# Performance work log

Hardware: AMD Instinct MI355X
Metric: run time of the kernel (lower is better)

The kernel has to match this reference:

```python
import jax, jax.numpy as jnp
import numpy as np

B, S, H = 64, 256, 1024


def setup_inputs() -> dict:
    key = jax.random.key(0)
    ks = jax.random.split(key, 16)
    f32 = jnp.float32

    def xavier(k, fan_in, fan_out):
        s = (2.0 / (fan_in + fan_out)) ** 0.5
        return jax.random.normal(k, (fan_in, fan_out), f32) * s

    return {
        "D": jax.random.normal(ks[0], (B, S, H), f32),
        "Q": jax.random.normal(ks[1], (B, 1, H), f32),
        "prev_mem": jax.random.normal(ks[2], (B, 1, H), f32),
        # AttnGRUCell params (weights stored [in, out])
        "Wr": xavier(ks[3], H, H), "br": jnp.zeros((H,), f32),
        "Ur": xavier(ks[4], H, H), "bur": jnp.zeros((H,), f32),
        "Wx": xavier(ks[5], H, H), "bx": jnp.zeros((H,), f32),
        "U": xavier(ks[6], H, H), "bu": jnp.zeros((H,), f32),
        # gate MLP
        "W1": xavier(ks[7], 4 * H, H), "b1": jnp.zeros((H,), f32),
        "W2": xavier(ks[8], H, 1), "b2": jnp.zeros((1,), f32),
        # memory update
        "Wm": xavier(ks[9], 3 * H, H), "bm": jnp.zeros((H,), f32),
    }


def reference(D, Q, prev_mem, Wr, br, Ur, bur, Wx, bx, U, bu, W1, b1, W2, b2, Wm, bm):
    # ----- gateMatrix: attention gate over sentences -----
    # z: [B, S, 4H]
    z = jnp.concatenate([D * Q, D * prev_mem, jnp.abs(D - Q), jnp.abs(D - prev_mem)], axis=-1)
    Zs = jnp.tanh(z @ W1 + b1) @ W2 + b2          # [B, S, 1]
    G = jax.nn.softmax(Zs[..., 0], axis=1)        # [B, S]

    # ----- AttnGRU: precompute input projections, scan over sentences -----
    Dr = D @ Wr + br                               # [B, S, H]
    Dw = D @ Wx + bx                               # [B, S, H]

    def step(h, t):
        dr, dw, g = t                              # dr,dw: [B,H]; g: [B]
        r = jax.nn.sigmoid(dr + h @ Ur + bur)
        h_tilda = jnp.tanh(dw + r * (h @ U + bu))
        g = g[:, None]
        h_new = g * h_tilda + (1.0 - g) * h
        return h_new, h_new

    h0 = jnp.zeros((D.shape[0], Ur.shape[0]), D.dtype)
    xs = (jnp.swapaxes(Dr, 0, 1), jnp.swapaxes(Dw, 0, 1), G.T)  # time-major
    C, hs = jax.lax.scan(step, h0, xs)
    hs = jnp.swapaxes(hs, 0, 1)                    # [B, S, H]

    # ----- memory update (dropout is identity in eval mode) -----
    concat = jnp.concatenate([prev_mem[:, 0, :], C, Q[:, 0, :]], axis=-1)  # [B, 3H]
    next_mem = jax.nn.relu(concat @ Wm + bm)[:, None, :]                    # [B, 1, H]
    return next_mem, hs
```

## Files before the change

### kernel.cpp

```cpp
#include <hip/hip_runtime.h>
#include <stdint.h>

typedef __bf16 bf16x8 __attribute__((ext_vector_type(8)));
typedef float f32x4 __attribute__((ext_vector_type(4)));

__device__ __forceinline__ float bf2f(unsigned short h) {
    union { unsigned int u; float f; } v; v.u = ((unsigned int)h) << 16; return v.f;
}
__device__ __forceinline__ unsigned short f2bf(float f) {
    union { float f; unsigned int u; } v; v.f = f;
    unsigned int r = (v.u + 0x7FFFu + ((v.u >> 16) & 1u)) >> 16;
    return (unsigned short)r;
}
__device__ __forceinline__ unsigned short f2bf_trunc(float f) {
    union { float f; unsigned int u; } v; v.f = f;
    return (unsigned short)(v.u >> 16);
}
__device__ __forceinline__ bf16x8 ldfrag(const unsigned short* p) {
    uint4 u = *(const uint4*)p; return __builtin_bit_cast(bf16x8, u);
}
__device__ __forceinline__ bf16x8 ldfrag_coh(const unsigned short* p) {
    union { unsigned long long q[2]; bf16x8 v; } u;
    u.q[0] = __hip_atomic_load((const unsigned long long*)p, __ATOMIC_RELAXED, __HIP_MEMORY_SCOPE_AGENT);
    u.q[1] = __hip_atomic_load((const unsigned long long*)(p + 4), __ATOMIC_RELAXED, __HIP_MEMORY_SCOPE_AGENT);
    return u.v;
}
__device__ __forceinline__ float fsigm(float x) { return 1.f / (1.f + __expf(-x)); }
__device__ __forceinline__ float ftanh(float x) { float e = __expf(2.f * x); return 1.f - 2.f / (e + 1.f); }

__global__ __launch_bounds__(256) void k_cast(const float* __restrict__ src,
                                              unsigned short* __restrict__ dst, int n4) {
    int i = blockIdx.x * 256 + threadIdx.x;
    if (i >= n4) return;
    float4 v = ((const float4*)src)[i];
    union { unsigned short s[4]; uint2 u; } o;
    o.s[0] = f2bf(v.x); o.s[1] = f2bf(v.y); o.s[2] = f2bf(v.z); o.s[3] = f2bf(v.w);
    ((uint2*)dst)[i] = o.u;
}

__global__ __launch_bounds__(256) void k_transpose_bf16(const float* __restrict__ src,
                                                        unsigned short* __restrict__ dst,
                                                        int R, int C) {
    __shared__ float tile[32][33];
    int tc = threadIdx.x & 31, tr = threadIdx.x >> 5;
    int r0 = blockIdx.y * 32, c0 = blockIdx.x * 32;
#pragma unroll
    for (int p = 0; p < 4; p++) tile[tr + p * 8][tc] = src[(size_t)(r0 + tr + p * 8) * C + c0 + tc];
    __syncthreads();
#pragma unroll
    for (int p = 0; p < 4; p++) dst[(size_t)(c0 + tr + p * 8) * R + r0 + tc] = f2bf(tile[tc][tr + p * 8]);
}

__global__ __launch_bounds__(256, 2) void k_gemm1(
    const unsigned short* __restrict__ Dc, const unsigned short* __restrict__ Qc,
    const unsigned short* __restrict__ Pc, const unsigned short* __restrict__ W1t,
    const float* __restrict__ b1, const float* __restrict__ W2, float* __restrict__ Zpart) {
    __shared__ alignas(16) unsigned short As[128][40];
    __shared__ alignas(16) unsigned short Bs[256][40];
    __shared__ float red[128];
    const int tid = threadIdx.x;
    const int nt = blockIdx.x, mt = blockIdx.y;
    const int r0 = mt * 128, n0 = nt * 256, b = r0 >> 8;
    const int lane = tid & 63, wid = tid >> 6;
    const int qm = wid & 1, qn = wid >> 1;
    const int nlane = lane & 15, quad = lane >> 4, k0 = quad * 8;

    f32x4 acc[4][8];
#pragma unroll
    for (int im = 0; im < 4; im++)
#pragma unroll
        for (int in = 0; in < 8; in++) acc[im][in] = (f32x4){0.f, 0.f, 0.f, 0.f};

    for (int kt = 0; kt < 128; ++kt) {
        const int q = kt >> 5;
        const int kq = (kt & 31) * 32;
        const unsigned short* wsrc = (q & 1) ? Pc : Qc;
#pragma unroll
        for (int rep = 0; rep < 2; ++rep) {
            int c = tid + rep * 256;
            int row = c >> 2, part = c & 3;
            uint4 d8 = *(const uint4*)(Dc + (size_t)(r0 + row) * 1024 + kq + part * 8);
            uint4 w8 = *(const uint4*)(wsrc + (size_t)b * 1024 + kq + part * 8);
            const unsigned short* d16 = (const unsigned short*)&d8;
            const unsigned short* w16 = (const unsigned short*)&w8;
            uint4 o; unsigned short* o16 = (unsigned short*)&o;
#pragma unroll
            for (int j = 0; j < 8; j++) {
                float dv = bf2f(d16[j]), wv = bf2f(w16[j]);
                float r = (q < 2) ? dv * wv : fabsf(dv - wv);
                o16[j] = f2bf_trunc(r);
            }
            *(uint4*)&As[row][part * 8] = o;
        }
#pragma unroll
        for (int rep = 0; rep < 4; ++rep) {
            int c = tid + rep * 256;
            int n = c >> 2, part = c & 3;
            *(uint4*)&Bs[n][part * 8] =
                *(const uint4*)(W1t + (size_t)(n0 + n) * 4096 + kt * 32 + part * 8);
        }
        __syncthreads();
        bf16x8 af[4], bfr[8];
#pragma unroll
        for (int im = 0; im < 4; im++) af[im] = ldfrag(&As[qm * 64 + im * 16 + nlane][k0]);
#pragma unroll
        for (int in = 0; in < 8; in++) bfr[in] = ldfrag(&Bs[qn * 128 + in * 16 + nlane][k0]);
#pragma unroll
        for (int im = 0; im < 4; im++)
#pragma unroll
            for (int in = 0; in < 8; in++)
                acc[im][in] = __builtin_amdgcn_mfma_f32_16x16x32_bf16(af[im], bfr[in], acc[im][in], 0, 0, 0);
        __syncthreads();
    }
    if (tid < 128) red[tid] = 0.f;
    __syncthreads();
    float b1v[8], w2v[8];
#pragma unroll
    for (int in = 0; in < 8; in++) {
        int col = n0 + qn * 128 + in * 16 + nlane;
        b1v[in] = b1[col]; w2v[in] = W2[col];
    }
#pragma unroll
    for (int im = 0; im < 4; im++)
#pragma unroll
        for (int i = 0; i < 4; i++) {
            float s = 0.f;
#pragma unroll
            for (int in = 0; in < 8; in++) s += ftanh(acc[im][in][i] + b1v[in]) * w2v[in];
            s += __shfl_xor(s, 1); s += __shfl_xor(s, 2); s += __shfl_xor(s, 4); s += __shfl_xor(s, 8);
            if (nlane == 0) atomicAdd(&red[qm * 64 + im * 16 + quad * 4 + i], s);
        }
    __syncthreads();
    if (tid < 128) Zpart[(size_t)(r0 + tid) * 4 + nt] = red[tid];
}

__global__ __launch_bounds__(256, 2) void k_gemm2(
    const unsigned short* __restrict__ Dc, const unsigned short* __restrict__ Wrxt,
    const float* __restrict__ br, const float* __restrict__ bx,
    unsigned short* __restrict__ Drwt) {
    __shared__ alignas(16) unsigned short As[128][40];
    __shared__ alignas(16) unsigned short Bs[256][40];
    const int tid = threadIdx.x;
    const int nt = blockIdx.x, mt = blockIdx.y;
    const int r0 = mt * 128, n0 = nt * 256;
    const int lane = tid & 63, wid = tid >> 6;
    const int qm = wid & 1, qn = wid >> 1;
    const int nlane = lane & 15, quad = lane >> 4, k0 = quad * 8;

    f32x4 acc[4][8];
#pragma unroll
    for (int im = 0; im < 4; im++)
#pragma unroll
        for (int in = 0; in < 8; in++) acc[im][in] = (f32x4){0.f, 0.f, 0.f, 0.f};

    for (int kt = 0; kt < 32; ++kt) {
#pragma unroll
        for (int rep = 0; rep < 2; ++rep) {
            int c = tid + rep * 256;
            int row = c >> 2, part = c & 3;
            *(uint4*)&As[row][part * 8] =
                *(const uint4*)(Dc + (size_t)(r0 + row) * 1024 + kt * 32 + part * 8);
        }
#pragma unroll
        for (int rep = 0; rep < 4; ++rep) {
            int c = tid + rep * 256;
            int n = c >> 2, part = c & 3;
            *(uint4*)&Bs[n][part * 8] =
                *(const uint4*)(Wrxt + (size_t)(n0 + n) * 1024 + kt * 32 + part * 8);
        }
        __syncthreads();
        bf16x8 af[4], bfr[8];
#pragma unroll
        for (int im = 0; im < 4; im++) af[im] = ldfrag(&As[qm * 64 + im * 16 + nlane][k0]);
#pragma unroll
        for (int in = 0; in < 8; in++) bfr[in] = ldfrag(&Bs[qn * 128 + in * 16 + nlane][k0]);
#pragma unroll
        for (int im = 0; im < 4; im++)
#pragma unroll
            for (int in = 0; in < 8; in++)
                acc[im][in] = __builtin_amdgcn_mfma_f32_16x16x32_bf16(af[im], bfr[in], acc[im][in], 0, 0, 0);
        __syncthreads();
    }
    float bias[8];
#pragma unroll
    for (int in = 0; in < 8; in++) {
        int col = n0 + qn * 128 + in * 16 + nlane;
        bias[in] = (col < 1024) ? br[col] : bx[col - 1024];
    }
#pragma unroll
    for (int im = 0; im < 4; im++)
#pragma unroll
        for (int i = 0; i < 4; i++) {
            int r = r0 + qm * 64 + im * 16 + quad * 4 + i;
            int bb = r >> 8, t = r & 255;
            unsigned short* dp = Drwt + ((size_t)t * 64 + bb) * 2048;
#pragma unroll
            for (int in = 0; in < 8; in++) {
                int col = n0 + qn * 128 + in * 16 + nlane;
                dp[col] = f2bf(acc[im][in][i] + bias[in]);
            }
        }
}

__global__ __launch_bounds__(256) void k_softmax(const float* __restrict__ Zpart,
                                                 float* __restrict__ Gt) {
    int b = blockIdx.x, s = threadIdx.x;
    const float* zp = Zpart + ((size_t)b * 256 + s) * 4;
    float l = zp[0] + zp[1] + zp[2] + zp[3];
    __shared__ float sm[4], ss[4];
    int lane = s & 63, wid = s >> 6;
    float m = l;
#pragma unroll
    for (int o = 32; o; o >>= 1) m = fmaxf(m, __shfl_xor(m, o));
    if (lane == 0) sm[wid] = m;
    __syncthreads();
    m = fmaxf(fmaxf(sm[0], sm[1]), fmaxf(sm[2], sm[3]));
    float e = __expf(l - m);
    float sum = e;
#pragma unroll
    for (int o = 32; o; o >>= 1) sum += __shfl_xor(sum, o);
    if (lane == 0) ss[wid] = sum;
    __syncthreads();
    sum = ss[0] + ss[1] + ss[2] + ss[3];
    Gt[(size_t)s * 64 + b] = e / sum;
}

__global__ __launch_bounds__(256, 1) void k_scan(
    const unsigned short* __restrict__ Urt, const unsigned short* __restrict__ Ut,
    const unsigned short* __restrict__ Drwt, const float* __restrict__ Gt,
    const float* __restrict__ bur, const float* __restrict__ bu,
    unsigned short* __restrict__ hb0, unsigned short* __restrict__ hb1,
    unsigned short* __restrict__ Cc, float* __restrict__ hs, int* __restrict__ flags) {
    const int w = blockIdx.x;
    const int tid = threadIdx.x, lane = tid & 63, wv = tid >> 6;
    const int nlane = lane & 15, quad = lane >> 4;
    const int n = w * 16 + nlane;
    const int m0 = wv * 16;
    const int brow = m0 + quad * 4;

    bf16x8 BU[32], BW[32];
#pragma unroll
    for (int ks = 0; ks < 32; ks++) {
        int kk = ks * 32 + quad * 8;
        BU[ks] = ldfrag(Urt + (size_t)n * 1024 + kk);
        BW[ks] = ldfrag(Ut + (size_t)n * 1024 + kk);
    }
    const float burj = bur[n], buj = bu[n];
    float hst[4] = {0.f, 0.f, 0.f, 0.f};
    const unsigned short* hcur = hb0;
    unsigned short* hnxt = hb1;

    float dr[4], dw[4], g[4];
#pragma unroll
    for (int i = 0; i < 4; i++) {
        int r = brow + i;
        const unsigned short* dp = Drwt + ((size_t)r) * 2048;
        dr[i] = bf2f(dp[n]);
        dw[i] = bf2f(dp[1024 + n]);
        g[i] = Gt[r];
    }

#pragma unroll 1
    for (int t = 0; t < 256; t++) {
        f32x4 aU0 = {0.f,0.f,0.f,0.f}, aU1 = {0.f,0.f,0.f,0.f};
        f32x4 aW0 = {0.f,0.f,0.f,0.f}, aW1 = {0.f,0.f,0.f,0.f};
        const unsigned short* hrow = hcur + (size_t)(m0 + nlane) * 1024 + quad * 8;
#pragma unroll
        for (int ks = 0; ks < 16; ks++) {
            bf16x8 a0 = ldfrag_coh(hrow + (2 * ks) * 32);
            bf16x8 a1 = ldfrag_coh(hrow + (2 * ks + 1) * 32);
            aU0 = __builtin_amdgcn_mfma_f32_16x16x32_bf16(a0, BU[2 * ks], aU0, 0, 0, 0);
            aW0 = __builtin_amdgcn_mfma_f32_16x16x32_bf16(a0, BW[2 * ks], aW0, 0, 0, 0);
            aU1 = __builtin_amdgcn_mfma_f32_16x16x32_bf16(a1, BU[2 * ks + 1], aU1, 0, 0, 0);
            aW1 = __builtin_amdgcn_mfma_f32_16x16x32_bf16(a1, BW[2 * ks + 1], aW1, 0, 0, 0);
        }
#pragma unroll
        for (int i = 0; i < 4; i++) {
            float r = fsigm(dr[i] + aU0[i] + aU1[i] + burj);
            float ht = ftanh(dw[i] + r * (aW0[i] + aW1[i] + buj));
            float hn = g[i] * ht + (1.f - g[i]) * hst[i];
            hst[i] = hn;
            int row = brow + i;
            __hip_atomic_store(&hnxt[(size_t)row * 1024 + n], f2bf(hn),
                               __ATOMIC_RELAXED, __HIP_MEMORY_SCOPE_AGENT);
            hs[((size_t)row * 256 + t) * 1024 + n] = hn;
        }
        if (t == 255) {
#pragma unroll
            for (int i = 0; i < 4; i++) Cc[(size_t)(brow + i) * 1024 + n] = f2bf(hst[i]);
        }
        __syncthreads();
        float drn[4], dwn[4], gn[4];
        if (t < 255) {
#pragma unroll
            for (int i = 0; i < 4; i++) {
                int r = brow + i;
                const unsigned short* dp = Drwt + ((size_t)(t + 1) * 64 + r) * 2048;
                drn[i] = bf2f(dp[n]);
                dwn[i] = bf2f(dp[1024 + n]);
                gn[i] = Gt[(t + 1) * 64 + r];
            }
            if (tid == 0)
                __hip_atomic_store(&flags[w], t + 1, __ATOMIC_RELAXED, __HIP_MEMORY_SCOPE_AGENT);
            if (tid < 64) {
                const int tgt = t + 1;
                while (true) {
                    int v = __hip_atomic_load(&flags[tid], __ATOMIC_RELAXED, __HIP_MEMORY_SCOPE_AGENT);
                    if (__ballot(v >= tgt) == ~0ull) break;
                }
            }
        }
        __syncthreads();
#pragma unroll
        for (int i = 0; i < 4; i++) { dr[i] = drn[i]; dw[i] = dwn[i]; g[i] = gn[i]; }
        const unsigned short* tmp = hcur; hcur = hnxt; hnxt = (unsigned short*)tmp;
    }
}

__global__ __launch_bounds__(256) void k_final(
    const unsigned short* __restrict__ Pc, const unsigned short* __restrict__ Cc,
    const unsigned short* __restrict__ Qc, const unsigned short* __restrict__ Wmt,
    const float* __restrict__ bm, float* __restrict__ outp) {
    __shared__ alignas(16) unsigned short As[64][40];
    __shared__ alignas(16) unsigned short Bs[128][40];
    const int tid = threadIdx.x;
    const int n0 = blockIdx.x * 128;
    const int lane = tid & 63, wid = tid >> 6;
    const int nlane = lane & 15, quad = lane >> 4, k0 = quad * 8;
    f32x4 acc[4][2];
#pragma unroll
    for (int im = 0; im < 4; im++) { acc[im][0] = (f32x4){0.f,0.f,0.f,0.f}; acc[im][1] = (f32x4){0.f,0.f,0.f,0.f}; }

    for (int kt = 0; kt < 96; ++kt) {
        {
            int row = tid >> 2, part = tid & 3;
            int kk = kt * 32 + part * 8;
            int sec = kk >> 10, off = kk & 1023;
            const unsigned short* sp = (sec == 0) ? Pc : (sec == 1) ? Cc : Qc;
            *(uint4*)&As[row][part * 8] = *(const uint4*)(sp + (size_t)row * 1024 + off);
        }
#pragma unroll
        for (int rep = 0; rep < 2; rep++) {
            int c = tid + rep * 256;
            int n = c >> 2, part = c & 3;
            *(uint4*)&Bs[n][part * 8] =
                *(const uint4*)(Wmt + (size_t)(n0 + n) * 3072 + kt * 32 + part * 8);
        }
        __syncthreads();
        bf16x8 af[4], bfr[2];
#pragma unroll
        for (int im = 0; im < 4; im++) af[im] = ldfrag(&As[im * 16 + nlane][k0]);
#pragma unroll
        for (int in = 0; in < 2; in++) bfr[in] = ldfrag(&Bs[wid * 32 + in * 16 + nlane][k0]);
#pragma unroll
        for (int im = 0; im < 4; im++)
#pragma unroll
            for (int in = 0; in < 2; in++)
                acc[im][in] = __builtin_amdgcn_mfma_f32_16x16x32_bf16(af[im], bfr[in], acc[im][in], 0, 0, 0);
        __syncthreads();
    }
#pragma unroll
    for (int im = 0; im < 4; im++)
#pragma unroll
        for (int i = 0; i < 4; i++)
#pragma unroll
            for (int in = 0; in < 2; in++) {
                int row = im * 16 + quad * 4 + i;
                int col = n0 + wid * 32 + in * 16 + nlane;
                float v = acc[im][in][i] + bm[col];
                outp[(size_t)row * 1024 + col] = fmaxf(v, 0.f);
            }
}

extern "C" void kernel_launch(void* const* d_in, const int* in_sizes, int n_in,
                              void* d_out, int out_size, void* d_ws, size_t ws_size,
                              hipStream_t stream) {
    const float* D  = (const float*)d_in[0];
    const float* Q  = (const float*)d_in[1];
    const float* P  = (const float*)d_in[2];
    const float* Wr = (const float*)d_in[3];
    const float* br = (const float*)d_in[4];
    const float* Ur = (const float*)d_in[5];
    const float* bur= (const float*)d_in[6];
    const float* Wx = (const float*)d_in[7];
    const float* bx = (const float*)d_in[8];
    const float* U  = (const float*)d_in[9];
    const float* bu = (const float*)d_in[10];
    const float* W1 = (const float*)d_in[11];
    const float* b1 = (const float*)d_in[12];
    const float* W2 = (const float*)d_in[13];
    const float* Wm = (const float*)d_in[15];
    const float* bm = (const float*)d_in[16];

    char* ws = (char*)d_ws;
    int* flags          = (int*)ws;
    unsigned short* hb0 = (unsigned short*)(ws + 256);
    unsigned short* hb1 = (unsigned short*)(ws + 131328);
    unsigned short* Dc  = (unsigned short*)(ws + 262400);
    unsigned short* Qc  = (unsigned short*)(ws + 33816832);
    unsigned short* Pc  = (unsigned short*)(ws + 33947904);
    unsigned short* W1t = (unsigned short*)(ws + 34078976);
    unsigned short* Wrxt= (unsigned short*)(ws + 42467584);
    unsigned short* Urt = (unsigned short*)(ws + 46661888);
    unsigned short* Utb = (unsigned short*)(ws + 48759040);
    unsigned short* Wmt = (unsigned short*)(ws + 50856192);
    unsigned short* Cc  = (unsigned short*)(ws + 57147648);
    float* Zpart        = (float*)(ws + 57278720);
    float* Gt           = (float*)(ws + 57540864);
    unsigned short* Drwt= (unsigned short*)(ws + 57606400);

    float* outNM = (float*)d_out;
    float* hsOut = (float*)d_out + 65536;

    hipMemsetAsync(ws, 0, 262400, stream);

    k_cast<<<16384, 256, 0, stream>>>(D, Dc, 4194304);
    k_cast<<<64, 256, 0, stream>>>(Q, Qc, 16384);
    k_cast<<<64, 256, 0, stream>>>(P, Pc, 16384);
    k_transpose_bf16<<<dim3(32, 128), 256, 0, stream>>>(W1, W1t, 4096, 1024);
    k_transpose_bf16<<<dim3(32, 32), 256, 0, stream>>>(Wr, Wrxt, 1024, 1024);
    k_transpose_bf16<<<dim3(32, 32), 256, 0, stream>>>(Wx, Wrxt + (size_t)1024 * 1024, 1024, 1024);
    k_transpose_bf16<<<dim3(32, 32), 256, 0, stream>>>(Ur, Urt, 1024, 1024);
    k_transpose_bf16<<<dim3(32, 32), 256, 0, stream>>>(U, Utb, 1024, 1024);
    k_transpose_bf16<<<dim3(32, 96), 256, 0, stream>>>(Wm, Wmt, 3072, 1024);

    k_gemm1<<<dim3(4, 128), 256, 0, stream>>>(Dc, Qc, Pc, W1t, b1, W2, Zpart);
    k_gemm2<<<dim3(8, 128), 256, 0, stream>>>(Dc, Wrxt, br, bx, Drwt);
    k_softmax<<<64, 256, 0, stream>>>(Zpart, Gt);
    k_scan<<<64, 256, 0, stream>>>(Urt, Utb, Drwt, Gt, bur, bu, hb0, hb1, Cc, hsOut, flags);
    k_final<<<8, 256, 0, stream>>>(Pc, Cc, Qc, Wmt, bm, outNM);
}
```

Before: 3.189 ms.

## Use per-timestep hidden-state buffers with non-coherent loads and lighter barrier in GRU scan

When the workspace is large enough, the scan writes each timestep's hidden state to its own buffer. Readers then use plain vector loads instead of agent-scope atomic loads, since no buffer is ever overwritten (no WAR hazard). The step also loads all hidden fragments up front before the MFMAs, and drops one __syncthreads by having every wave poll the flags itself. The risk is stale data from plain cached loads, which depends on caches not holding old lines. A `dep` term is added to stop the compiler reordering loads across the spin.

```diff
diff --git a/kernel.cpp b/kernel.cpp
--- a/kernel.cpp
+++ b/kernel.cpp
@@ -225,11 +225,12 @@
     Gt[(size_t)s * 64 + b] = e / sum;
 }
 
+template <int BIG>
 __global__ __launch_bounds__(256, 1) void k_scan(
     const unsigned short* __restrict__ Urt, const unsigned short* __restrict__ Ut,
     const unsigned short* __restrict__ Drwt, const float* __restrict__ Gt,
     const float* __restrict__ bur, const float* __restrict__ bu,
-    unsigned short* __restrict__ hb0, unsigned short* __restrict__ hb1,
+    unsigned short* __restrict__ hb,
     unsigned short* __restrict__ Cc, float* __restrict__ hs, int* __restrict__ flags) {
     const int w = blockIdx.x;
     const int tid = threadIdx.x, lane = tid & 63, wv = tid >> 6;
@@ -247,33 +248,37 @@
     }
     const float burj = bur[n], buj = bu[n];
     float hst[4] = {0.f, 0.f, 0.f, 0.f};
-    const unsigned short* hcur = hb0;
-    unsigned short* hnxt = hb1;
+    size_t dep = 0;
 
     float dr[4], dw[4], g[4];
 #pragma unroll
     for (int i = 0; i < 4; i++) {
         int r = brow + i;
-        const unsigned short* dp = Drwt + ((size_t)r) * 2048;
-        dr[i] = bf2f(dp[n]);
-        dw[i] = bf2f(dp[1024 + n]);
-        g[i] = Gt[r];
+        const unsigned short* dp = Drwt + (size_t)r * 2048;
+        dr[i] = bf2f(dp[n]); dw[i] = bf2f(dp[1024 + n]); g[i] = Gt[r];
     }
 
 #pragma unroll 1
     for (int t = 0; t < 256; t++) {
+        const unsigned short* hcur = hb + (((size_t)(BIG ? t : (t & 1))) << 16) + dep;
+        unsigned short* hnxt = hb + (((size_t)(BIG ? (t + 1) : ((t + 1) & 1))) << 16);
+        const unsigned short* hrow = hcur + (size_t)(m0 + nlane) * 1024 + quad * 8;
+
+        bf16x8 hf[32];
+#pragma unroll
+        for (int ks = 0; ks < 32; ks++)
+            hf[ks] = BIG ? ldfrag(hrow + ks * 32) : ldfrag_coh(hrow + ks * 32);
+
         f32x4 aU0 = {0.f,0.f,0.f,0.f}, aU1 = {0.f,0.f,0.f,0.f};
         f32x4 aW0 = {0.f,0.f,0.f,0.f}, aW1 = {0.f,0.f,0.f,0.f};
-        const unsigned short* hrow = hcur + (size_t)(m0 + nlane) * 1024 + quad * 8;
-#pragma unroll
-        for (int ks = 0; ks < 16; ks++) {
-            bf16x8 a0 = ldfrag_coh(hrow + (2 * ks) * 32);
-            bf16x8 a1 = ldfrag_coh(hrow + (2 * ks + 1) * 32);
-            aU0 = __builtin_amdgcn_mfma_f32_16x16x32_bf16(a0, BU[2 * ks], aU0, 0, 0, 0);
-            aW0 = __builtin_amdgcn_mfma_f32_16x16x32_bf16(a0, BW[2 * ks], aW0, 0, 0, 0);
-            aU1 = __builtin_amdgcn_mfma_f32_16x16x32_bf16(a1, BU[2 * ks + 1], aU1, 0, 0, 0);
-            aW1 = __builtin_amdgcn_mfma_f32_16x16x32_bf16(a1, BW[2 * ks + 1], aW1, 0, 0, 0);
-        }
+#pragma unroll
+        for (int ks = 0; ks < 32; ks += 2) {
+            aU0 = __builtin_amdgcn_mfma_f32_16x16x32_bf16(hf[ks], BU[ks], aU0, 0, 0, 0);
+            aW0 = __builtin_amdgcn_mfma_f32_16x16x32_bf16(hf[ks], BW[ks], aW0, 0, 0, 0);
+            aU1 = __builtin_amdgcn_mfma_f32_16x16x32_bf16(hf[ks + 1], BU[ks + 1], aU1, 0, 0, 0);
+            aW1 = __builtin_amdgcn_mfma_f32_16x16x32_bf16(hf[ks + 1], BW[ks + 1], aW1, 0, 0, 0);
+        }
+
 #pragma unroll
         for (int i = 0; i < 4; i++) {
             float r = fsigm(dr[i] + aU0[i] + aU1[i] + burj);
@@ -281,39 +286,34 @@
             float hn = g[i] * ht + (1.f - g[i]) * hst[i];
             hst[i] = hn;
             int row = brow + i;
-            __hip_atomic_store(&hnxt[(size_t)row * 1024 + n], f2bf(hn),
-                               __ATOMIC_RELAXED, __HIP_MEMORY_SCOPE_AGENT);
+            if (t < 255)
+                __hip_atomic_store(&hnxt[(size_t)row * 1024 + n], f2bf(hn),
+                                   __ATOMIC_RELAXED, __HIP_MEMORY_SCOPE_AGENT);
             hs[((size_t)row * 256 + t) * 1024 + n] = hn;
         }
         if (t == 255) {
 #pragma unroll
             for (int i = 0; i < 4; i++) Cc[(size_t)(brow + i) * 1024 + n] = f2bf(hst[i]);
-        }
-        __syncthreads();
-        float drn[4], dwn[4], gn[4];
-        if (t < 255) {
+        } else {
+            float drn[4], dwn[4], gn[4];
 #pragma unroll
             for (int i = 0; i < 4; i++) {
                 int r = brow + i;
                 const unsigned short* dp = Drwt + ((size_t)(t + 1) * 64 + r) * 2048;
-                drn[i] = bf2f(dp[n]);
-                dwn[i] = bf2f(dp[1024 + n]);
-                gn[i] = Gt[(t + 1) * 64 + r];
+                drn[i] = bf2f(dp[n]); dwn[i] = bf2f(dp[1024 + n]); gn[i] = Gt[(t + 1) * 64 + r];
             }
+            __syncthreads();
             if (tid == 0)
                 __hip_atomic_store(&flags[w], t + 1, __ATOMIC_RELAXED, __HIP_MEMORY_SCOPE_AGENT);
-            if (tid < 64) {
-                const int tgt = t + 1;
-                while (true) {
-                    int v = __hip_atomic_load(&flags[tid], __ATOMIC_RELAXED, __HIP_MEMORY_SCOPE_AGENT);
-                    if (__ballot(v >= tgt) == ~0ull) break;
-                }
-            }
-        }
-        __syncthreads();
-#pragma unroll
-        for (int i = 0; i < 4; i++) { dr[i] = drn[i]; dw[i] = dwn[i]; g[i] = gn[i]; }
-        const unsigned short* tmp = hcur; hcur = hnxt; hnxt = (unsigned short*)tmp;
+            const int tgt = t + 1;
+            int myv;
+            do {
+                myv = __hip_atomic_load(&flags[lane], __ATOMIC_RELAXED, __HIP_MEMORY_SCOPE_AGENT);
+            } while (__ballot(myv >= tgt) != ~0ull);
+            dep += (myv >= tgt) ? 0 : 1;
+#pragma unroll
+            for (int i = 0; i < 4; i++) { dr[i] = drn[i]; dw[i] = dwn[i]; g[i] = gn[i]; }
+        }
     }
 }
 
@@ -393,26 +393,35 @@
     const float* bm = (const float*)d_in[16];
 
     char* ws = (char*)d_ws;
-    int* flags          = (int*)ws;
-    unsigned short* hb0 = (unsigned short*)(ws + 256);
-    unsigned short* hb1 = (unsigned short*)(ws + 131328);
-    unsigned short* Dc  = (unsigned short*)(ws + 262400);
-    unsigned short* Qc  = (unsigned short*)(ws + 33816832);
-    unsigned short* Pc  = (unsigned short*)(ws + 33947904);
-    unsigned short* W1t = (unsigned short*)(ws + 34078976);
-    unsigned short* Wrxt= (unsigned short*)(ws + 42467584);
-    unsigned short* Urt = (unsigned short*)(ws + 46661888);
-    unsigned short* Utb = (unsigned short*)(ws + 48759040);
-    unsigned short* Wmt = (unsigned short*)(ws + 50856192);
-    unsigned short* Cc  = (unsigned short*)(ws + 57147648);
-    float* Zpart        = (float*)(ws + 57278720);
-    float* Gt           = (float*)(ws + 57540864);
-    unsigned short* Drwt= (unsigned short*)(ws + 57606400);
+    const size_t HB_BIG = 33554432ull;
+    const size_t HB_SMALL = 262144ull;
+    const size_t SZ_Dc = 33554432, SZ_Qc = 131072, SZ_Pc = 131072, SZ_W1t = 8388608,
+                 SZ_Wrxt = 4194304, SZ_Urt = 2097152, SZ_Utb = 2097152, SZ_Wmt = 6291456,
+                 SZ_Cc = 131072, SZ_Zp = 262144, SZ_Gt = 65536, SZ_Drwt = 67108864;
+    const size_t common = SZ_Dc + SZ_Qc + SZ_Pc + SZ_W1t + SZ_Wrxt + SZ_Urt + SZ_Utb +
+                          SZ_Wmt + SZ_Cc + SZ_Zp + SZ_Gt + SZ_Drwt;
+    const bool big = ws_size >= 4096 + HB_BIG + common;
+
+    size_t cur = 0;
+    int* flags          = (int*)(ws + cur);            cur += 4096;
+    unsigned short* hb  = (unsigned short*)(ws + cur); cur += big ? HB_BIG : HB_SMALL;
+    unsigned short* Dc  = (unsigned short*)(ws + cur); cur += SZ_Dc;
+    unsigned short* Qc  = (unsigned short*)(ws + cur); cur += SZ_Qc;
+    unsigned short* Pc  = (unsigned short*)(ws + cur); cur += SZ_Pc;
+    unsigned short* W1t = (unsigned short*)(ws + cur); cur += SZ_W1t;
+    unsigned short* Wrxt= (unsigned short*)(ws + cur); cur += SZ_Wrxt;
+    unsigned short* Urt = (unsigned short*)(ws + cur); cur += SZ_Urt;
+    unsigned short* Utb = (unsigned short*)(ws + cur); cur += SZ_Utb;
+    unsigned short* Wmt = (unsigned short*)(ws + cur); cur += SZ_Wmt;
+    unsigned short* Cc  = (unsigned short*)(ws + cur); cur += SZ_Cc;
+    float* Zpart        = (float*)(ws + cur);          cur += SZ_Zp;
+    float* Gt           = (float*)(ws + cur);          cur += SZ_Gt;
+    unsigned short* Drwt= (unsigned short*)(ws + cur); cur += SZ_Drwt;
 
     float* outNM = (float*)d_out;
     float* hsOut = (float*)d_out + 65536;
 
-    hipMemsetAsync(ws, 0, 262400, stream);
+    hipMemsetAsync(ws, 0, 4096 + 131072, stream);
 
     k_cast<<<16384, 256, 0, stream>>>(D, Dc, 4194304);
     k_cast<<<64, 256, 0, stream>>>(Q, Qc, 16384);
@@ -427,6 +436,9 @@
     k_gemm1<<<dim3(4, 128), 256, 0, stream>>>(Dc, Qc, Pc, W1t, b1, W2, Zpart);
     k_gemm2<<<dim3(8, 128), 256, 0, stream>>>(Dc, Wrxt, br, bx, Drwt);
     k_softmax<<<64, 256, 0, stream>>>(Zpart, Gt);
-    k_scan<<<64, 256, 0, stream>>>(Urt, Utb, Drwt, Gt, bur, bu, hb0, hb1, Cc, hsOut, flags);
+    if (big)
+        k_scan<1><<<64, 256, 0, stream>>>(Urt, Utb, Drwt, Gt, bur, bu, hb, Cc, hsOut, flags);
+    else
+        k_scan<0><<<64, 256, 0, stream>>>(Urt, Utb, Drwt, Gt, bur, bu, hb, Cc, hsOut, flags);
     k_final<<<8, 256, 0, stream>>>(Pc, Cc, Qc, Wmt, bm, outNM);
 }
```

Result: faster. 3.072 ms (-3.7%).
